# Optimization experiments

Measured on AMD Instinct MI355X. Metric: run time of the kernel, lower is better.

## Reference

```python
import jax, jax.numpy as jnp
import numpy as np

D_MODEL = 1024
N_HEADS = 16
D_HEAD = D_MODEL // N_HEADS
B, S = 4, 2048
NEG_INF = float('-inf')


def setup_inputs() -> dict:
    key = jax.random.key(0)
    ks = jax.random.split(key, 12)
    sc = 1.0 / np.sqrt(D_MODEL)
    inp = {
        'query': jax.random.normal(ks[0], (B, S, D_MODEL), jnp.float32),
        'key': jax.random.normal(ks[1], (B, S, D_MODEL), jnp.float32),
        'value': jax.random.normal(ks[2], (B, S, D_MODEL), jnp.float32),
        'mask': jnp.ones((B, S), jnp.int32),
        'W_q': jax.random.normal(ks[3], (D_MODEL, D_MODEL), jnp.float32) * sc,
        'b_q': jax.random.normal(ks[4], (D_MODEL,), jnp.float32) * sc,
        'W_k': jax.random.normal(ks[5], (D_MODEL, D_MODEL), jnp.float32) * sc,
        'b_k': jax.random.normal(ks[6], (D_MODEL,), jnp.float32) * sc,
        'W_v': jax.random.normal(ks[7], (D_MODEL, D_MODEL), jnp.float32) * sc,
        'b_v': jax.random.normal(ks[8], (D_MODEL,), jnp.float32) * sc,
        'W_o': jax.random.normal(ks[9], (D_MODEL, D_MODEL), jnp.float32) * sc,
        'b_o': jax.random.normal(ks[10], (D_MODEL,), jnp.float32) * sc,
    }
    return inp


def reference(query, key, value, mask, W_q, b_q, W_k, b_k, W_v, b_v, W_o, b_o):
    b, s, d = query.shape
    # QKV projections, split heads: [B,S,D] -> [B,H,S,Dh]
    def proj(x, W, bias):
        y = x @ W + bias
        return y.reshape(b, s, N_HEADS, D_HEAD).transpose(0, 2, 1, 3)
    q = proj(query, W_q, b_q)
    k = proj(key, W_k, b_k)
    v = proj(value, W_v, b_v)
    # NOTE: original scales by d_head**2 (not sqrt) — kept faithful.
    e = jnp.einsum('bhqd,bhkd->bhqk', q, k) / (D_HEAD ** 2)
    # key padding mask: [B,S] -> additive [B,1,1,S]
    pad = jnp.where(mask == 0, NEG_INF, 0.0).astype(e.dtype)[:, None, None, :]
    e = e + pad
    # causal mask: additive lower-triangular
    causal = jnp.where(jnp.tril(jnp.ones((s, s), bool)), 0.0, NEG_INF).astype(e.dtype)
    e = e + causal[None, None, :, :]
    a = jax.nn.softmax(e, axis=-1)
    c = jnp.einsum('bhqk,bhkd->bhqd', a, v)  # [B,H,S,Dh]
    c = c.transpose(0, 2, 1, 3).reshape(b, s, d)
    return c @ W_o + b_o
```

## Files before the change

### kernel.cpp

```cpp
#include <hip/hip_runtime.h>

typedef __bf16 bf16;
typedef unsigned int u32;
typedef float f32x4 __attribute__((ext_vector_type(4)));
typedef __bf16 bf16x4 __attribute__((ext_vector_type(4)));
typedef __bf16 bf16x8 __attribute__((ext_vector_type(8)));

#define MFMA(a, b, c) __builtin_amdgcn_mfma_f32_16x16x32_bf16((a), (b), (c), 0, 0, 0)

static constexpr int Bc = 4;
static constexpr int Sc = 2048;
static constexpr int Hc = 16;
static constexpr int DHc = 64;
static constexpr int Dc = 1024;
static constexpr int Mc = Bc * Sc;

__device__ __forceinline__ void load_lds16(const bf16* gp, bf16* lp) {
    __builtin_amdgcn_global_load_lds(
        reinterpret_cast<const __attribute__((address_space(1))) u32*>(
            reinterpret_cast<uintptr_t>(gp)),
        reinterpret_cast<__attribute__((address_space(3))) u32*>(
            static_cast<u32>(reinterpret_cast<uintptr_t>(lp))),
        16, 0, 0);
}

__global__ void fill_diag(float* out, int n) {
    int i = blockIdx.x * 256 + threadIdx.x;
    if (i < n) out[i] = 1000.0f;
}

__global__ __launch_bounds__(256) void cvt_bf16(const float* __restrict__ in,
                                                bf16* __restrict__ out, int n) {
    int i = (blockIdx.x * 256 + threadIdx.x) * 8;
    if (i < n) {
        f32x4 a = *(const f32x4*)&in[i];
        f32x4 b = *(const f32x4*)&in[i + 4];
        bf16x8 v;
#pragma unroll
        for (int j = 0; j < 4; ++j) { v[j] = (bf16)a[j]; v[j + 4] = (bf16)b[j]; }
        *(bf16x8*)&out[i] = v;
    }
}

__global__ __launch_bounds__(256) void transpose4(
    const float* __restrict__ A0, const float* __restrict__ A1,
    const float* __restrict__ A2, const float* __restrict__ A3,
    bf16* __restrict__ O0, bf16* __restrict__ O1,
    bf16* __restrict__ O2, bf16* __restrict__ O3) {
    __shared__ bf16 t[32][33];
    const float* in = blockIdx.z == 0 ? A0 : blockIdx.z == 1 ? A1
                    : blockIdx.z == 2 ? A2 : A3;
    bf16* out = blockIdx.z == 0 ? O0 : blockIdx.z == 1 ? O1
              : blockIdx.z == 2 ? O2 : O3;
    int x = blockIdx.x * 32 + threadIdx.x;
#pragma unroll
    for (int j = 0; j < 32; j += 8) {
        int y = blockIdx.y * 32 + threadIdx.y + j;
        t[threadIdx.y + j][threadIdx.x] = (bf16)in[y * 1024 + x];
    }
    __syncthreads();
    int x2 = blockIdx.y * 32 + threadIdx.x;
#pragma unroll
    for (int j = 0; j < 32; j += 8) {
        int y2 = blockIdx.x * 32 + threadIdx.y + j;
        out[y2 * 1024 + x2] = t[threadIdx.x][threadIdx.y + j];
    }
}

template <int MODE, typename TOUT>
__global__ __launch_bounds__(256) void gemm_bt(const bf16* __restrict__ A,
                                               const bf16* __restrict__ Wt,
                                               const float* __restrict__ bias,
                                               TOUT* __restrict__ out,
                                               int M, int N, int K) {
    __shared__ alignas(16) bf16 As[128 * 32];
    __shared__ alignas(16) bf16 Bs[128 * 32];
    const int tid = threadIdx.x;
    const int wave = tid >> 6, lane = tid & 63;
    const int quad = lane >> 4, l16 = lane & 15;
    const int wr = (wave >> 1) * 64, wc = (wave & 1) * 64;
    const int id = blockIdx.y * 8 + blockIdx.x;
    const int sw = (id & 7) * 64 + (id >> 3);
    const int row0 = (sw >> 3) * 128, col0 = (sw & 7) * 128;

    const int sr = wave * 32 + (lane >> 2);
    const int sk = (lane & 3) * 8;
    const bf16* gA = &A[(size_t)(row0 + sr) * K + sk];
    const bf16* gB = &Wt[(size_t)(col0 + sr) * K + sk];
    bf16* lA = &As[wave * 32 * 32];
    bf16* lB = &Bs[wave * 32 * 32];

    f32x4 acc[4][4];
#pragma unroll
    for (int mi = 0; mi < 4; ++mi)
#pragma unroll
        for (int ni = 0; ni < 4; ++ni)
            acc[mi][ni] = (f32x4){0.f, 0.f, 0.f, 0.f};

    for (int k0 = 0; k0 < K; k0 += 32) {
        __syncthreads();
        load_lds16(gA + k0, lA);
        load_lds16(gA + k0 + 16 * K, lA + 16 * 32);
        load_lds16(gB + k0, lB);
        load_lds16(gB + k0 + 16 * K, lB + 16 * 32);
        __syncthreads();

        bf16x8 af[4], bf_[4];
#pragma unroll
        for (int mi = 0; mi < 4; ++mi)
            af[mi] = *(const bf16x8*)&As[(wr + mi * 16 + l16) * 32 + quad * 8];
#pragma unroll
        for (int ni = 0; ni < 4; ++ni)
            bf_[ni] = *(const bf16x8*)&Bs[(wc + ni * 16 + l16) * 32 + quad * 8];
#pragma unroll
        for (int mi = 0; mi < 4; ++mi)
#pragma unroll
            for (int ni = 0; ni < 4; ++ni)
                acc[mi][ni] = MFMA(af[mi], bf_[ni], acc[mi][ni]);
    }

#pragma unroll
    for (int mi = 0; mi < 4; ++mi) {
#pragma unroll
        for (int ni = 0; ni < 4; ++ni) {
            int col = col0 + wc + ni * 16 + l16;
            float bv = bias[col];
#pragma unroll
            for (int r = 0; r < 4; ++r) {
                int row = row0 + wr + mi * 16 + quad * 4 + r;
                float v = acc[mi][ni][r] + bv;
                size_t off;
                if (MODE == 0) {
                    off = (size_t)row * N + col;
                } else {
                    int b = row >> 11, s = row & (Sc - 1);
                    int h = col >> 6, dh = col & (DHc - 1);
                    if (MODE == 1)
                        off = (((size_t)(b * Hc + h) * Sc + s) << 6) + dh;
                    else
                        off = (((size_t)(b * Hc + h) * DHc + dh) << 11) + s;
                }
                out[off] = (TOUT)v;
            }
        }
    }
}

static constexpr int LPP = 72;
static constexpr float CEXP = 1.4426950408889634f / 4096.0f;

__global__ __launch_bounds__(256, 2) void attn_fwd(const bf16* __restrict__ Q,
                                                   const bf16* __restrict__ K,
                                                   const bf16* __restrict__ Vt,
                                                   const int* __restrict__ mask,
                                                   bf16* __restrict__ Ctx) {
    __shared__ alignas(16) bf16 Ks[2][64 * 64];
    __shared__ alignas(16) bf16 Vs[2][64 * 64];
    __shared__ alignas(16) bf16 Ps[4][32 * LPP];
    __shared__ alignas(16) float msk_all[Sc];

    const int tid = threadIdx.x;
    const int wave = tid >> 6, lane = tid & 63;
    const int quad = lane >> 4, l16 = lane & 15;
    const int id = blockIdx.y * 8 + blockIdx.x;
    const int sw = (id & 7) * 64 + (id >> 3);
    const int bh = sw >> 3, p = sw & 7;
    const int b = bh >> 4, h = bh & 15;

    {
        const int i = tid * 8;
        int4 m0 = *(const int4*)&mask[b * Sc + i];
        int4 m1 = *(const int4*)&mask[b * Sc + i + 4];
        f32x4 f0 = {m0.x ? 0.f : -1e30f, m0.y ? 0.f : -1e30f,
                    m0.z ? 0.f : -1e30f, m0.w ? 0.f : -1e30f};
        f32x4 f1 = {m1.x ? 0.f : -1e30f, m1.y ? 0.f : -1e30f,
                    m1.z ? 0.f : -1e30f, m1.w ? 0.f : -1e30f};
        *(f32x4*)&msk_all[i] = f0;
        *(f32x4*)&msk_all[i + 4] = f1;
    }

    const int swz = ((lane & 7) ^ (lane >> 3)) << 4;
    const int rA = wave * 16 + (lane >> 3);
    const char* gK0 = (const char*)K + (size_t)bh * Sc * (DHc * 2)
                    + (size_t)rA * 128 + swz;
    const char* gV0 = (const char*)Vt + (size_t)bh * DHc * (Sc * 2)
                    + (size_t)rA * (Sc * 2) + swz;
    bf16* lK0 = &Ks[0][(wave * 16) * 64];
    bf16* lV0 = &Vs[0][(wave * 16) * 64];

    const int m7 = l16 & 7;
    const int gsw0 = ((0 + quad) ^ m7) * 8;
    const int gsw1 = ((4 + quad) ^ m7) * 8;

#define STAGE(BUF, KB)                                                        \
    do {                                                                      \
        load_lds16((const bf16*)(gK0 + (size_t)(KB) * 128),                   \
                   lK0 + (BUF) * (64 * 64));                                  \
        load_lds16((const bf16*)(gK0 + (size_t)(KB) * 128 + 1024),            \
                   lK0 + (BUF) * (64 * 64) + 8 * 64);                         \
        load_lds16((const bf16*)(gV0 + (size_t)(KB) * 2),                     \
                   lV0 + (BUF) * (64 * 64));                                  \
        load_lds16((const bf16*)(gV0 + (size_t)(KB) * 2 + 8 * 4096),          \
                   lV0 + (BUF) * (64 * 64) + 8 * 64);                         \
    } while (0)

#pragma unroll 1
    for (int pass = 0; pass < 2; ++pass) {
        const int qt = pass ? p : 15 - p;
        const int qr0 = qt * 128 + wave * 32;
        const int qmax = qr0 + 31;

        bf16x8 bq[2][2];
#pragma unroll
        for (int mt = 0; mt < 2; ++mt) {
            const size_t qoff = ((size_t)bh * Sc + qr0 + mt * 16 + l16) * DHc;
            bq[mt][0] = *(const bf16x8*)&Q[qoff + quad * 8];
            bq[mt][1] = *(const bf16x8*)&Q[qoff + 32 + quad * 8];
        }

        f32x4 accO[2][4];
#pragma unroll
        for (int mt = 0; mt < 2; ++mt)
#pragma unroll
            for (int oi = 0; oi < 4; ++oi) accO[mt][oi] = (f32x4){0.f, 0.f, 0.f, 0.f};
        float l_part[2] = {0.f, 0.f};

        const int nkt = 2 * qt + 2;
        STAGE(0, 0);
        __syncthreads();
        int cur = 0;
#pragma unroll 1
        for (int kt = 0; kt < nkt; ++kt) {
            const int kb = kt * 64;
            if (kt + 1 < nkt) STAGE(cur ^ 1, kb + 64);
            if (kb <= qmax) {
                const bf16* Kb_ = &Ks[cur][0];
                const bf16* Vb_ = &Vs[cur][0];

                f32x4 st[2][4];
                __builtin_amdgcn_s_setprio(1);
#pragma unroll
                for (int kti = 0; kti < 4; ++kti) {
                    bf16x8 ak0 = *(const bf16x8*)&Kb_[(kti * 16 + l16) * 64 + gsw0];
                    bf16x8 ak1 = *(const bf16x8*)&Kb_[(kti * 16 + l16) * 64 + gsw1];
#pragma unroll
                    for (int mt = 0; mt < 2; ++mt) {
                        f32x4 z = {0.f, 0.f, 0.f, 0.f};
                        z = MFMA(ak0, bq[mt][0], z);
                        z = MFMA(ak1, bq[mt][1], z);
                        st[mt][kti] = z;
                    }
                }
                __builtin_amdgcn_s_setprio(0);

#define SM_TILE(DIAG)                                                          \
                _Pragma("unroll")                                              \
                for (int mt = 0; mt < 2; ++mt) {                               \
                    _Pragma("unroll")                                          \
                    for (int kti = 0; kti < 4; ++kti) {                        \
                        const f32x4 mkv =                                      \
                            *(const f32x4*)&msk_all[kb + kti * 16 + quad * 4]; \
                        const int cbase =                                      \
                            kb + kti * 16 + quad * 4 - (qr0 + mt * 16);        \
                        bf16x4 pv;                                             \
                        _Pragma("unroll")                                      \
                        for (int r = 0; r < 4; ++r) {                          \
                            float s = st[mt][kti][r] * CEXP + mkv[r];          \
                            if (DIAG) s = (cbase + r > l16) ? -1e30f : s;      \
                            float p_ = __builtin_amdgcn_exp2f(s);              \
                            l_part[mt] += p_;                                  \
                            pv[r] = (bf16)p_;                                  \
                        }                                                      \
                        *(bf16x4*)&Ps[wave][(mt * 16 + l16) * LPP +            \
                                            kti * 16 + quad * 4] = pv;         \
                    }                                                          \
                }
                if (kb + 63 > qr0) { SM_TILE(1) } else { SM_TILE(0) }
#undef SM_TILE

                __builtin_amdgcn_s_setprio(1);
#pragma unroll
                for (int kk = 0; kk < 2; ++kk) {
                    bf16x8 ap0 = *(const bf16x8*)&Ps[wave][(l16) * LPP + kk * 32 + quad * 8];
                    bf16x8 ap1 = *(const bf16x8*)&Ps[wave][(16 + l16) * LPP + kk * 32 + quad * 8];
                    const int vg = kk ? gsw1 : gsw0;
#pragma unroll
                    for (int oi = 0; oi < 4; ++oi) {
                        bf16x8 bv = *(const bf16x8*)&Vb_[(oi * 16 + l16) * 64 + vg];
                        accO[0][oi] = MFMA(ap0, bv, accO[0][oi]);
                        accO[1][oi] = MFMA(ap1, bv, accO[1][oi]);
                    }
                }
                __builtin_amdgcn_s_setprio(0);
            }
            asm volatile("s_waitcnt vmcnt(0)" ::: "memory");
            __builtin_amdgcn_s_barrier();
            __builtin_amdgcn_sched_barrier(0);
            cur ^= 1;
        }

        float lvi[2][4];
#pragma unroll
        for (int mt = 0; mt < 2; ++mt) {
            float l = l_part[mt];
            l += __shfl_xor(l, 16);
            l += __shfl_xor(l, 32);
#pragma unroll
            for (int r = 0; r < 4; ++r)
                lvi[mt][r] = __builtin_amdgcn_rcpf(__shfl(l, quad * 4 + r));
        }
#pragma unroll
        for (int mt = 0; mt < 2; ++mt)
#pragma unroll
            for (int oi = 0; oi < 4; ++oi)
#pragma unroll
                for (int r = 0; r < 4; ++r) {
                    int s = qr0 + mt * 16 + quad * 4 + r;
                    int dh = oi * 16 + l16;
                    float v = accO[mt][oi][r] * lvi[mt][r];
                    Ctx[((size_t)b * Sc + s) * Dc + h * DHc + dh] = (bf16)v;
                }
    }
#undef STAGE
}

extern "C" void kernel_launch(void* const* d_in, const int* in_sizes, int n_in,
                              void* d_out, int out_size, void* d_ws, size_t ws_size,
                              hipStream_t stream) {
    const float* query = (const float*)d_in[0];
    const float* key_i = (const float*)d_in[1];
    const float* value = (const float*)d_in[2];
    const int* mask    = (const int*)d_in[3];
    const float* W_q = (const float*)d_in[4];
    const float* b_q = (const float*)d_in[5];
    const float* W_k = (const float*)d_in[6];
    const float* b_k = (const float*)d_in[7];
    const float* W_v = (const float*)d_in[8];
    const float* b_v = (const float*)d_in[9];
    const float* W_o = (const float*)d_in[10];
    const float* b_o = (const float*)d_in[11];
    float* out = (float*)d_out;

    const size_t MB = 1024 * 1024;
    const size_t NEED = 72 * MB;
    if (ws_size < NEED) {
        fill_diag<<<(out_size + 255) / 256, 256, 0, stream>>>(out, out_size);
        return;
    }

    char* ws = (char*)d_ws;
    bf16* WtQ = (bf16*)(ws + 0 * MB);
    bf16* WtK = (bf16*)(ws + 2 * MB);
    bf16* WtV = (bf16*)(ws + 4 * MB);
    bf16* WtO = (bf16*)(ws + 6 * MB);
    bf16* Xin = (bf16*)(ws + 8 * MB);
    bf16* Ctx = (bf16*)(ws + 8 * MB);
    bf16* Qb  = (bf16*)(ws + 24 * MB);
    bf16* Kb  = (bf16*)(ws + 40 * MB);
    bf16* Vtb = (bf16*)(ws + 56 * MB);

    transpose4<<<dim3(32, 32, 4), dim3(32, 8), 0, stream>>>(
        W_q, W_k, W_v, W_o, WtQ, WtK, WtV, WtO);

    const int ncv = Mc * Dc;
    dim3 gg(Dc / 128, Mc / 128);

    cvt_bf16<<<ncv / (256 * 8), 256, 0, stream>>>(query, Xin, ncv);
    gemm_bt<1, bf16><<<gg, 256, 0, stream>>>(Xin, WtQ, b_q, Qb, Mc, Dc, Dc);
    cvt_bf16<<<ncv / (256 * 8), 256, 0, stream>>>(key_i, Xin, ncv);
    gemm_bt<1, bf16><<<gg, 256, 0, stream>>>(Xin, WtK, b_k, Kb, Mc, Dc, Dc);
    cvt_bf16<<<ncv / (256 * 8), 256, 0, stream>>>(value, Xin, ncv);
    gemm_bt<2, bf16><<<gg, 256, 0, stream>>>(Xin, WtV, b_v, Vtb, Mc, Dc, Dc);

    attn_fwd<<<dim3(8, Bc * Hc), 256, 0, stream>>>(Qb, Kb, Vtb, mask, Ctx);

    gemm_bt<0, float><<<gg, 256, 0, stream>>>(Ctx, WtO, b_o, out, Mc, Dc, Dc);
}
```

Measured before the change: 346.4 us.

## Fuse fp32-to-bf16 conversion into a batched QKV GEMM and split attention per query tile

Removes the three standalone fp32-to-bf16 conversion kernels. The Q, K and V projections become one launch (grid z=3) that loads fp32 activations, converts them in registers and writes them to LDS. The attention kernel now gives each block a single 128-row query tile instead of two balanced passes, streams the mask per key tile through a small LDS buffer instead of staging the whole row, swizzles the P buffer instead of padding it, and raises the occupancy hint to 3. This cuts launches and intermediate traffic, but the fused GEMM uses synchronous global loads for A with no prefetch, and per-block work in attention is now imbalanced across the causal triangle.

Measured after the change: 377.1 us. 1.09x slower.

```diff
diff --git a/kernel.cpp b/kernel.cpp
--- a/kernel.cpp
+++ b/kernel.cpp
@@ -27,19 +27,6 @@
 __global__ void fill_diag(float* out, int n) {
     int i = blockIdx.x * 256 + threadIdx.x;
     if (i < n) out[i] = 1000.0f;
-}
-
-__global__ __launch_bounds__(256) void cvt_bf16(const float* __restrict__ in,
-                                                bf16* __restrict__ out, int n) {
-    int i = (blockIdx.x * 256 + threadIdx.x) * 8;
-    if (i < n) {
-        f32x4 a = *(const f32x4*)&in[i];
-        f32x4 b = *(const f32x4*)&in[i + 4];
-        bf16x8 v;
-#pragma unroll
-        for (int j = 0; j < 4; ++j) { v[j] = (bf16)a[j]; v[j + 4] = (bf16)b[j]; }
-        *(bf16x8*)&out[i] = v;
-    }
 }
 
 __global__ __launch_bounds__(256) void transpose4(
@@ -67,11 +54,105 @@
     }
 }
 
-template <int MODE, typename TOUT>
+__global__ __launch_bounds__(256) void gemm_qkv(
+    const float* __restrict__ Aq, const float* __restrict__ Ak,
+    const float* __restrict__ Av,
+    const bf16* __restrict__ Wq, const bf16* __restrict__ Wk,
+    const bf16* __restrict__ Wv,
+    const float* __restrict__ bq, const float* __restrict__ bk,
+    const float* __restrict__ bv,
+    bf16* __restrict__ Oq, bf16* __restrict__ Ok, bf16* __restrict__ Ov) {
+    __shared__ alignas(16) bf16 As[4 * 128 * 8];
+    __shared__ alignas(16) bf16 Bs[128 * 32];
+    const int z = blockIdx.z;
+    const float* A = z == 0 ? Aq : z == 1 ? Ak : Av;
+    const bf16* Wt = z == 0 ? Wq : z == 1 ? Wk : Wv;
+    const float* bias = z == 0 ? bq : z == 1 ? bk : bv;
+    bf16* out = z == 0 ? Oq : z == 1 ? Ok : Ov;
+    const bool vmode = (z == 2);
+
+    const int tid = threadIdx.x;
+    const int wave = tid >> 6, lane = tid & 63;
+    const int quad = lane >> 4, l16 = lane & 15;
+    const int wr = (wave >> 1) * 64, wc = (wave & 1) * 64;
+    const int id = blockIdx.y * 8 + blockIdx.x;
+    const int sw = (id & 7) * 64 + (id >> 3);
+    const int row0 = (sw >> 3) * 128, col0 = (sw & 7) * 128;
+
+    const int rw = wave * 32 + (lane >> 1);
+    const int ce = (lane & 1) * 2;
+    const float* gA = &A[(size_t)(row0 + rw) * Dc + ce * 8];
+    const int sr = wave * 32 + (lane >> 2);
+    const int sk = (lane & 3) * 8;
+    const bf16* gB = &Wt[(size_t)(col0 + sr) * Dc + sk];
+    bf16* lB = &Bs[wave * 32 * 32];
+
+    f32x4 acc[4][4];
+#pragma unroll
+    for (int mi = 0; mi < 4; ++mi)
+#pragma unroll
+        for (int ni = 0; ni < 4; ++ni)
+            acc[mi][ni] = (f32x4){0.f, 0.f, 0.f, 0.f};
+
+    for (int k0 = 0; k0 < Dc; k0 += 32) {
+        __syncthreads();
+        f32x4 a0 = *(const f32x4*)(gA + k0);
+        f32x4 a1 = *(const f32x4*)(gA + k0 + 4);
+        f32x4 a2 = *(const f32x4*)(gA + k0 + 8);
+        f32x4 a3 = *(const f32x4*)(gA + k0 + 12);
+        load_lds16(gB + k0, lB);
+        load_lds16(gB + k0 + 16 * Dc, lB + 16 * 32);
+        bf16x8 v0, v1;
+#pragma unroll
+        for (int j = 0; j < 4; ++j) {
+            v0[j] = (bf16)a0[j]; v0[j + 4] = (bf16)a1[j];
+            v1[j] = (bf16)a2[j]; v1[j + 4] = (bf16)a3[j];
+        }
+        *(bf16x8*)&As[ce * 1024 + rw * 8] = v0;
+        *(bf16x8*)&As[(ce + 1) * 1024 + rw * 8] = v1;
+        __syncthreads();
+
+        bf16x8 af[4], bf_[4];
+#pragma unroll
+        for (int mi = 0; mi < 4; ++mi)
+            af[mi] = *(const bf16x8*)&As[quad * 1024 + (wr + mi * 16 + l16) * 8];
+#pragma unroll
+        for (int ni = 0; ni < 4; ++ni)
+            bf_[ni] = *(const bf16x8*)&Bs[(wc + ni * 16 + l16) * 32 + quad * 8];
+#pragma unroll
+        for (int mi = 0; mi < 4; ++mi)
+#pragma unroll
+            for (int ni = 0; ni < 4; ++ni)
+                acc[mi][ni] = MFMA(af[mi], bf_[ni], acc[mi][ni]);
+    }
+
+#pragma unroll
+    for (int mi = 0; mi < 4; ++mi) {
+#pragma unroll
+        for (int ni = 0; ni < 4; ++ni) {
+            int col = col0 + wc + ni * 16 + l16;
+            float bv = bias[col];
+#pragma unroll
+            for (int r = 0; r < 4; ++r) {
+                int row = row0 + wr + mi * 16 + quad * 4 + r;
+                float v = acc[mi][ni][r] + bv;
+                int b = row >> 11, s = row & (Sc - 1);
+                int h = col >> 6, dh = col & (DHc - 1);
+                size_t off;
+                if (!vmode)
+                    off = (((size_t)(b * Hc + h) * Sc + s) << 6) + dh;
+                else
+                    off = (((size_t)(b * Hc + h) * DHc + dh) << 11) + s;
+                out[off] = (bf16)v;
+            }
+        }
+    }
+}
+
 __global__ __launch_bounds__(256) void gemm_bt(const bf16* __restrict__ A,
                                                const bf16* __restrict__ Wt,
                                                const float* __restrict__ bias,
-                                               TOUT* __restrict__ out,
+                                               float* __restrict__ out,
                                                int M, int N, int K) {
     __shared__ alignas(16) bf16 As[128 * 32];
     __shared__ alignas(16) bf16 Bs[128 * 32];
@@ -128,56 +209,33 @@
 #pragma unroll
             for (int r = 0; r < 4; ++r) {
                 int row = row0 + wr + mi * 16 + quad * 4 + r;
-                float v = acc[mi][ni][r] + bv;
-                size_t off;
-                if (MODE == 0) {
-                    off = (size_t)row * N + col;
-                } else {
-                    int b = row >> 11, s = row & (Sc - 1);
-                    int h = col >> 6, dh = col & (DHc - 1);
-                    if (MODE == 1)
-                        off = (((size_t)(b * Hc + h) * Sc + s) << 6) + dh;
-                    else
-                        off = (((size_t)(b * Hc + h) * DHc + dh) << 11) + s;
-                }
-                out[off] = (TOUT)v;
+                out[(size_t)row * N + col] = acc[mi][ni][r] + bv;
             }
         }
     }
 }
 
-static constexpr int LPP = 72;
 static constexpr float CEXP = 1.4426950408889634f / 4096.0f;
 
-__global__ __launch_bounds__(256, 2) void attn_fwd(const bf16* __restrict__ Q,
+__global__ __launch_bounds__(256, 3) void attn_fwd(const bf16* __restrict__ Q,
                                                    const bf16* __restrict__ K,
                                                    const bf16* __restrict__ Vt,
                                                    const int* __restrict__ mask,
                                                    bf16* __restrict__ Ctx) {
     __shared__ alignas(16) bf16 Ks[2][64 * 64];
     __shared__ alignas(16) bf16 Vs[2][64 * 64];
-    __shared__ alignas(16) bf16 Ps[4][32 * LPP];
-    __shared__ alignas(16) float msk_all[Sc];
+    __shared__ alignas(16) bf16 Ps[4][32 * 64];
+    __shared__ alignas(16) float msk[2][64];
 
     const int tid = threadIdx.x;
     const int wave = tid >> 6, lane = tid & 63;
     const int quad = lane >> 4, l16 = lane & 15;
-    const int id = blockIdx.y * 8 + blockIdx.x;
-    const int sw = (id & 7) * 64 + (id >> 3);
-    const int bh = sw >> 3, p = sw & 7;
-    const int b = bh >> 4, h = bh & 15;
-
-    {
-        const int i = tid * 8;
-        int4 m0 = *(const int4*)&mask[b * Sc + i];
-        int4 m1 = *(const int4*)&mask[b * Sc + i + 4];
-        f32x4 f0 = {m0.x ? 0.f : -1e30f, m0.y ? 0.f : -1e30f,
-                    m0.z ? 0.f : -1e30f, m0.w ? 0.f : -1e30f};
-        f32x4 f1 = {m1.x ? 0.f : -1e30f, m1.y ? 0.f : -1e30f,
-                    m1.z ? 0.f : -1e30f, m1.w ? 0.f : -1e30f};
-        *(f32x4*)&msk_all[i] = f0;
-        *(f32x4*)&msk_all[i + 4] = f1;
-    }
+    const int id = blockIdx.y * 16 + blockIdx.x;
+    const int sw = (id & 7) * 128 + (id >> 3);
+    const int bh = sw >> 4, b = bh >> 4, h = bh & 15;
+    const int qt = 15 - (sw & 15);
+    const int qr0 = qt * 128 + wave * 32;
+    const int qmax = qr0 + 31;
 
     const int swz = ((lane & 7) ^ (lane >> 3)) << 4;
     const int rA = wave * 16 + (lane >> 3);
@@ -204,124 +262,130 @@
                    lV0 + (BUF) * (64 * 64) + 8 * 64);                         \
     } while (0)
 
+    bf16x8 bq[2][2];
+#pragma unroll
+    for (int mt = 0; mt < 2; ++mt) {
+        const size_t qoff = ((size_t)bh * Sc + qr0 + mt * 16 + l16) * DHc;
+        bq[mt][0] = *(const bf16x8*)&Q[qoff + quad * 8];
+        bq[mt][1] = *(const bf16x8*)&Q[qoff + 32 + quad * 8];
+    }
+
+    f32x4 accO[2][4];
+#pragma unroll
+    for (int mt = 0; mt < 2; ++mt)
+#pragma unroll
+        for (int oi = 0; oi < 4; ++oi) accO[mt][oi] = (f32x4){0.f, 0.f, 0.f, 0.f};
+    float l_part[2] = {0.f, 0.f};
+
+    const int nkt = 2 * qt + 2;
+    int mreg = 1;
+    if (tid < 64) {
+        msk[0][tid] = mask[b * Sc + tid] ? 0.f : -1e30f;
+        mreg = mask[b * Sc + 64 + tid];
+    }
+    STAGE(0, 0);
+    __syncthreads();
+    int cur = 0;
 #pragma unroll 1
-    for (int pass = 0; pass < 2; ++pass) {
-        const int qt = pass ? p : 15 - p;
-        const int qr0 = qt * 128 + wave * 32;
-        const int qmax = qr0 + 31;
-
-        bf16x8 bq[2][2];
-#pragma unroll
-        for (int mt = 0; mt < 2; ++mt) {
-            const size_t qoff = ((size_t)bh * Sc + qr0 + mt * 16 + l16) * DHc;
-            bq[mt][0] = *(const bf16x8*)&Q[qoff + quad * 8];
-            bq[mt][1] = *(const bf16x8*)&Q[qoff + 32 + quad * 8];
+    for (int kt = 0; kt < nkt; ++kt) {
+        const int kb = kt * 64;
+        if (kt + 1 < nkt) {
+            STAGE(cur ^ 1, kb + 64);
+            if (tid < 64) {
+                msk[cur ^ 1][tid] = mreg ? 0.f : -1e30f;
+                mreg = mask[b * Sc + ((kb + 128 + tid) & (Sc - 1))];
+            }
         }
-
-        f32x4 accO[2][4];
-#pragma unroll
-        for (int mt = 0; mt < 2; ++mt)
-#pragma unroll
-            for (int oi = 0; oi < 4; ++oi) accO[mt][oi] = (f32x4){0.f, 0.f, 0.f, 0.f};
-        float l_part[2] = {0.f, 0.f};
-
-        const int nkt = 2 * qt + 2;
-        STAGE(0, 0);
-        __syncthreads();
-        int cur = 0;
-#pragma unroll 1
-        for (int kt = 0; kt < nkt; ++kt) {
-            const int kb = kt * 64;
-            if (kt + 1 < nkt) STAGE(cur ^ 1, kb + 64);
-            if (kb <= qmax) {
-                const bf16* Kb_ = &Ks[cur][0];
-                const bf16* Vb_ = &Vs[cur][0];
-
-                f32x4 st[2][4];
-                __builtin_amdgcn_s_setprio(1);
-#pragma unroll
-                for (int kti = 0; kti < 4; ++kti) {
-                    bf16x8 ak0 = *(const bf16x8*)&Kb_[(kti * 16 + l16) * 64 + gsw0];
-                    bf16x8 ak1 = *(const bf16x8*)&Kb_[(kti * 16 + l16) * 64 + gsw1];
-#pragma unroll
-                    for (int mt = 0; mt < 2; ++mt) {
-                        f32x4 z = {0.f, 0.f, 0.f, 0.f};
-                        z = MFMA(ak0, bq[mt][0], z);
-                        z = MFMA(ak1, bq[mt][1], z);
-                        st[mt][kti] = z;
-                    }
+        if (kb <= qmax) {
+            const bf16* Kb_ = &Ks[cur][0];
+            const bf16* Vb_ = &Vs[cur][0];
+
+            f32x4 st[2][4];
+            __builtin_amdgcn_s_setprio(1);
+#pragma unroll
+            for (int kti = 0; kti < 4; ++kti) {
+                bf16x8 ak0 = *(const bf16x8*)&Kb_[(kti * 16 + l16) * 64 + gsw0];
+                bf16x8 ak1 = *(const bf16x8*)&Kb_[(kti * 16 + l16) * 64 + gsw1];
+#pragma unroll
+                for (int mt = 0; mt < 2; ++mt) {
+                    f32x4 z = {0.f, 0.f, 0.f, 0.f};
+                    z = MFMA(ak0, bq[mt][0], z);
+                    z = MFMA(ak1, bq[mt][1], z);
+                    st[mt][kti] = z;
                 }
-                __builtin_amdgcn_s_setprio(0);
+            }
+            __builtin_amdgcn_s_setprio(0);
 
 #define SM_TILE(DIAG)                                                          \
+            _Pragma("unroll")                                                  \
+            for (int mt = 0; mt < 2; ++mt) {                                   \
                 _Pragma("unroll")                                              \
-                for (int mt = 0; mt < 2; ++mt) {                               \
+                for (int kti = 0; kti < 4; ++kti) {                            \
+                    const f32x4 mkv =                                          \
+                        *(const f32x4*)&msk[cur][kti * 16 + quad * 4];         \
+                    const int cbase =                                          \
+                        kb + kti * 16 + quad * 4 - (qr0 + mt * 16);            \
+                    bf16x4 pv;                                                 \
                     _Pragma("unroll")                                          \
-                    for (int kti = 0; kti < 4; ++kti) {                        \
-                        const f32x4 mkv =                                      \
-                            *(const f32x4*)&msk_all[kb + kti * 16 + quad * 4]; \
-                        const int cbase =                                      \
-                            kb + kti * 16 + quad * 4 - (qr0 + mt * 16);        \
-                        bf16x4 pv;                                             \
-                        _Pragma("unroll")                                      \
-                        for (int r = 0; r < 4; ++r) {                          \
-                            float s = st[mt][kti][r] * CEXP + mkv[r];          \
-                            if (DIAG) s = (cbase + r > l16) ? -1e30f : s;      \
-                            float p_ = __builtin_amdgcn_exp2f(s);              \
-                            l_part[mt] += p_;                                  \
-                            pv[r] = (bf16)p_;                                  \
-                        }                                                      \
-                        *(bf16x4*)&Ps[wave][(mt * 16 + l16) * LPP +            \
-                                            kti * 16 + quad * 4] = pv;         \
+                    for (int r = 0; r < 4; ++r) {                              \
+                        float s = st[mt][kti][r] * CEXP + mkv[r];              \
+                        if (DIAG) s = (cbase + r > l16) ? -1e30f : s;          \
+                        float p_ = __builtin_amdgcn_exp2f(s);                  \
+                        l_part[mt] += p_;                                      \
+                        pv[r] = (bf16)p_;                                      \
                     }                                                          \
+                    *(bf16x4*)&Ps[wave][(mt * 16 + l16) * 64 +                 \
+                        (((kti * 2 + (quad >> 1)) ^ m7) * 8) +                 \
+                        (quad & 1) * 4] = pv;                                  \
+                }                                                              \
+            }
+            if (kb + 63 > qr0) { SM_TILE(1) } else { SM_TILE(0) }
+#undef SM_TILE
+
+            __builtin_amdgcn_s_setprio(1);
+#pragma unroll
+            for (int kk = 0; kk < 2; ++kk) {
+                const int pg = ((kk * 4 + quad) ^ m7) * 8;
+                bf16x8 ap0 = *(const bf16x8*)&Ps[wave][(l16) * 64 + pg];
+                bf16x8 ap1 = *(const bf16x8*)&Ps[wave][(16 + l16) * 64 + pg];
+                const int vg = kk ? gsw1 : gsw0;
+#pragma unroll
+                for (int oi = 0; oi < 4; ++oi) {
+                    bf16x8 bv = *(const bf16x8*)&Vb_[(oi * 16 + l16) * 64 + vg];
+                    accO[0][oi] = MFMA(ap0, bv, accO[0][oi]);
+                    accO[1][oi] = MFMA(ap1, bv, accO[1][oi]);
                 }
-                if (kb + 63 > qr0) { SM_TILE(1) } else { SM_TILE(0) }
-#undef SM_TILE
-
-                __builtin_amdgcn_s_setprio(1);
-#pragma unroll
-                for (int kk = 0; kk < 2; ++kk) {
-                    bf16x8 ap0 = *(const bf16x8*)&Ps[wave][(l16) * LPP + kk * 32 + quad * 8];
-                    bf16x8 ap1 = *(const bf16x8*)&Ps[wave][(16 + l16) * LPP + kk * 32 + quad * 8];
-                    const int vg = kk ? gsw1 : gsw0;
-#pragma unroll
-                    for (int oi = 0; oi < 4; ++oi) {
-                        bf16x8 bv = *(const bf16x8*)&Vb_[(oi * 16 + l16) * 64 + vg];
-                        accO[0][oi] = MFMA(ap0, bv, accO[0][oi]);
-                        accO[1][oi] = MFMA(ap1, bv, accO[1][oi]);
-                    }
-                }
-                __builtin_amdgcn_s_setprio(0);
-            }
-            asm volatile("s_waitcnt vmcnt(0)" ::: "memory");
-            __builtin_amdgcn_s_barrier();
-            __builtin_amdgcn_sched_barrier(0);
-            cur ^= 1;
+            }
+            __builtin_amdgcn_s_setprio(0);
         }
-
-        float lvi[2][4];
-#pragma unroll
-        for (int mt = 0; mt < 2; ++mt) {
-            float l = l_part[mt];
-            l += __shfl_xor(l, 16);
-            l += __shfl_xor(l, 32);
-#pragma unroll
-            for (int r = 0; r < 4; ++r)
-                lvi[mt][r] = __builtin_amdgcn_rcpf(__shfl(l, quad * 4 + r));
-        }
-#pragma unroll
-        for (int mt = 0; mt < 2; ++mt)
-#pragma unroll
-            for (int oi = 0; oi < 4; ++oi)
-#pragma unroll
-                for (int r = 0; r < 4; ++r) {
-                    int s = qr0 + mt * 16 + quad * 4 + r;
-                    int dh = oi * 16 + l16;
-                    float v = accO[mt][oi][r] * lvi[mt][r];
-                    Ctx[((size_t)b * Sc + s) * Dc + h * DHc + dh] = (bf16)v;
-                }
+        asm volatile("s_waitcnt vmcnt(0) lgkmcnt(0)" ::: "memory");
+        __builtin_amdgcn_s_barrier();
+        __builtin_amdgcn_sched_barrier(0);
+        cur ^= 1;
     }
 #undef STAGE
+
+    float lvi[2][4];
+#pragma unroll
+    for (int mt = 0; mt < 2; ++mt) {
+        float l = l_part[mt];
+        l += __shfl_xor(l, 16);
+        l += __shfl_xor(l, 32);
+#pragma unroll
+        for (int r = 0; r < 4; ++r)
+            lvi[mt][r] = __builtin_amdgcn_rcpf(__shfl(l, quad * 4 + r));
+    }
+#pragma unroll
+    for (int mt = 0; mt < 2; ++mt)
+#pragma unroll
+        for (int oi = 0; oi < 4; ++oi)
+#pragma unroll
+            for (int r = 0; r < 4; ++r) {
+                int s = qr0 + mt * 16 + quad * 4 + r;
+                int dh = oi * 16 + l16;
+                float v = accO[mt][oi][r] * lvi[mt][r];
+                Ctx[((size_t)b * Sc + s) * Dc + h * DHc + dh] = (bf16)v;
+            }
 }
 
 extern "C" void kernel_launch(void* const* d_in, const int* in_sizes, int n_in,
@@ -353,26 +417,18 @@
     bf16* WtK = (bf16*)(ws + 2 * MB);
     bf16* WtV = (bf16*)(ws + 4 * MB);
     bf16* WtO = (bf16*)(ws + 6 * MB);
-    bf16* Xin = (bf16*)(ws + 8 * MB);
-    bf16* Ctx = (bf16*)(ws + 8 * MB);
-    bf16* Qb  = (bf16*)(ws + 24 * MB);
-    bf16* Kb  = (bf16*)(ws + 40 * MB);
-    bf16* Vtb = (bf16*)(ws + 56 * MB);
+    bf16* Qb  = (bf16*)(ws + 8 * MB);
+    bf16* Kb  = (bf16*)(ws + 24 * MB);
+    bf16* Vtb = (bf16*)(ws + 40 * MB);
+    bf16* Ctx = (bf16*)(ws + 56 * MB);
 
     transpose4<<<dim3(32, 32, 4), dim3(32, 8), 0, stream>>>(
         W_q, W_k, W_v, W_o, WtQ, WtK, WtV, WtO);
 
-    const int ncv = Mc * Dc;
-    dim3 gg(Dc / 128, Mc / 128);
-
-    cvt_bf16<<<ncv / (256 * 8), 256, 0, stream>>>(query, Xin, ncv);
-    gemm_bt<1, bf16><<<gg, 256, 0, stream>>>(Xin, WtQ, b_q, Qb, Mc, Dc, Dc);
-    cvt_bf16<<<ncv / (256 * 8), 256, 0, stream>>>(key_i, Xin, ncv);
-    gemm_bt<1, bf16><<<gg, 256, 0, stream>>>(Xin, WtK, b_k, Kb, Mc, Dc, Dc);
-    cvt_bf16<<<ncv / (256 * 8), 256, 0, stream>>>(value, Xin, ncv);
-    gemm_bt<2, bf16><<<gg, 256, 0, stream>>>(Xin, WtV, b_v, Vtb, Mc, Dc, Dc);
-
-    attn_fwd<<<dim3(8, Bc * Hc), 256, 0, stream>>>(Qb, Kb, Vtb, mask, Ctx);
-
-    gemm_bt<0, float><<<gg, 256, 0, stream>>>(Ctx, WtO, b_o, out, Mc, Dc, Dc);
-}
+    gemm_qkv<<<dim3(8, 64, 3), 256, 0, stream>>>(
+        query, key_i, value, WtQ, WtK, WtV, b_q, b_k, b_v, Qb, Kb, Vtb);
+
+    attn_fwd<<<dim3(16, 64), 256, 0, stream>>>(Qb, Kb, Vtb, mask, Ctx);
+
+    gemm_bt<<<dim3(8, 64), 256, 0, stream>>>(Ctx, WtO, b_o, out, Mc, Dc, Dc);
+}
```
